# Kernel optimization log

Hardware: AMD Instinct MI355X
Metric: run time of the kernel (lower is better)

Reference implementation:

```python
import jax, jax.numpy as jnp
import numpy as np

N_USERS = 100000
N_ITEMS = 50000
D = 64
L = 3          # TopKformer_layers
E = 1000000    # number of train (user,item) edges


def setup_inputs() -> dict:
    key = jax.random.key(0)
    k1, k2, k3, k4, k5 = jax.random.split(key, 5)
    return {
        "users_w": jax.random.normal(k1, (N_USERS, D), jnp.float32) * 0.1,
        "items_w": jax.random.normal(k2, (N_ITEMS, D), jnp.float32) * 0.1,
        "beta_w": jax.random.normal(k3, (N_USERS, L), jnp.float32),
        "train_user": jax.random.randint(k4, (E,), 0, N_USERS, dtype=jnp.int32),
        "train_item": jax.random.randint(k5, (E,), 0, N_ITEMS, dtype=jnp.int32),
    }


def reference(users_w, items_w, beta_w, train_user, train_item):
    """Model.computer(): LightGCN-style bipartite propagation where each
    layer's user update is gated by a learned per-user beta = tanh(beta_w).
    Returns concat([user_embs, item_embs]) after L propagation layers."""
    beta = jnp.tanh(beta_w)  # [N_USERS, L], as in Model.beta_value

    # symmetric degree normalization 1/sqrt(d_u * d_i) over train edges
    ones = jnp.ones(train_user.shape[0], users_w.dtype)
    du = jnp.clip(jax.ops.segment_sum(ones, train_user, N_USERS), 1.0)
    di = jnp.clip(jax.ops.segment_sum(ones, train_item, N_ITEMS), 1.0)
    norm = (1.0 / jnp.sqrt(du[train_user] * di[train_item]))[:, None]  # [E,1]

    u_emb, i_emb = users_w, items_w
    for l in range(L):
        # gather neighbor embeddings along edges, scatter-add back (irregular access)
        msg_u = jax.ops.segment_sum(i_emb[train_item] * norm, train_user, N_USERS)
        msg_i = jax.ops.segment_sum(u_emb[train_user] * norm, train_item, N_ITEMS)
        u_emb = msg_u + beta[:, l:l + 1] * u_emb  # beta-weighted residual (per user)
        i_emb = msg_i
    return jnp.concatenate([u_emb, i_emb], axis=0)  # [N_USERS+N_ITEMS, D]
```

## Files before the change

kernel.cpp:

```cpp
#include <hip/hip_runtime.h>

#define NUSERS 100000
#define NITEMS 50000
#define NV (NUSERS + NITEMS)
#define DIM 64
#define NLAYERS 3
#define PAD 64
#define BINSHIFT 9
#define BINSZ 512
#define NBINS ((NV + BINSZ - 1) / BINSZ)
#define EPB 1024

typedef _Float16 half4v __attribute__((ext_vector_type(4)));
typedef _Float16 half8v __attribute__((ext_vector_type(8)));

__global__ void hist_kernel(const int* __restrict__ tu, const int* __restrict__ ti,
                            int* __restrict__ cnt, int E) {
    __shared__ int h[NBINS];
    int t = threadIdx.x, b = blockIdx.x;
    for (int i = t; i < NBINS; i += 256) h[i] = 0;
    __syncthreads();
    int base = b * EPB;
#pragma unroll
    for (int j = 0; j < 4; ++j) {
        int e = base + t + 256 * j;
        if (e < E) {
            atomicAdd(&h[tu[e] >> BINSHIFT], 1);
            atomicAdd(&h[(NUSERS + ti[e]) >> BINSHIFT], 1);
        }
    }
    __syncthreads();
    for (int i = t; i < NBINS; i += 256) cnt[(size_t)b * NBINS + i] = h[i];
}

__global__ void colscan_kernel(int* __restrict__ cnt, int* __restrict__ bintot, int nblk) {
    __shared__ int sh[256];
    int bin = blockIdx.x, t = threadIdx.x;
    int chunk = (nblk + 255) / 256;
    int v[8];
    int sum = 0;
    for (int j = 0; j < chunk; ++j) {
        int blk = t * chunk + j;
        v[j] = (blk < nblk) ? cnt[(size_t)blk * NBINS + bin] : 0;
        sum += v[j];
    }
    sh[t] = sum;
    __syncthreads();
    for (int d = 1; d < 256; d <<= 1) {
        int x = (t >= d) ? sh[t - d] : 0;
        __syncthreads();
        sh[t] += x;
        __syncthreads();
    }
    int run = sh[t] - sum;
    for (int j = 0; j < chunk; ++j) {
        int blk = t * chunk + j;
        if (blk < nblk) { cnt[(size_t)blk * NBINS + bin] = run; run += v[j]; }
    }
    if (t == 255) bintot[bin] = sh[255];
}

__global__ void binscan_kernel(const int* __restrict__ bintot, int* __restrict__ binstart) {
    __shared__ int sh[512];
    int t = threadIdx.x;
    int v = (t < NBINS) ? bintot[t] : 0;
    sh[t] = v;
    __syncthreads();
    for (int d = 1; d < 512; d <<= 1) {
        int x = (t >= d) ? sh[t - d] : 0;
        __syncthreads();
        sh[t] += x;
        __syncthreads();
    }
    if (t < NBINS) binstart[t] = sh[t] - v;
    if (t == NBINS - 1) binstart[NBINS] = sh[t];
}

__global__ void scatter_kernel(const int* __restrict__ tu, const int* __restrict__ ti,
                               const int* __restrict__ cnt, const int* __restrict__ binstart,
                               unsigned int* __restrict__ binbuf, int E) {
    __shared__ int h[NBINS];
    __shared__ int bb[NBINS];
    __shared__ int bs[NBINS];
    int t = threadIdx.x, b = blockIdx.x;
    for (int i = t; i < NBINS; i += 256) {
        h[i] = 0;
        bb[i] = cnt[(size_t)b * NBINS + i];
        bs[i] = binstart[i];
    }
    __syncthreads();
    int base = b * EPB;
#pragma unroll
    for (int j = 0; j < 4; ++j) {
        int e = base + t + 256 * j;
        if (e < E) {
            int u = tu[e];
            int w = NUSERS + ti[e];
            int bu = u >> BINSHIFT, bw = w >> BINSHIFT;
            int r1 = atomicAdd(&h[bu], 1);
            int r2 = atomicAdd(&h[bw], 1);
            binbuf[bs[bu] + bb[bu] + r1] = ((unsigned)(u & (BINSZ - 1)) << 18) | (unsigned)w;
            binbuf[bs[bw] + bb[bw] + r2] = ((unsigned)(w & (BINSZ - 1)) << 18) | (unsigned)u;
        }
    }
}

__global__ void bfill_kernel(const unsigned int* __restrict__ binbuf,
                             const int* __restrict__ binstart,
                             int* __restrict__ deg, int* __restrict__ adj) {
    __shared__ int c[BINSZ];
    int bin = blockIdx.x, t = threadIdx.x;
    c[t] = 0;
    __syncthreads();
    int start = binstart[bin];
    int n = binstart[bin + 1] - start;
    int vbase = bin << BINSHIFT;
    for (int k = t; k < n; k += 512) {
        unsigned rec = binbuf[start + k];
        int vloc = rec >> 18;
        int nbr = (int)(rec & 0x3FFFFu);
        int r = atomicAdd(&c[vloc], 1);
        adj[((vbase + vloc) << 6) + r] = nbr << 7;
    }
    __syncthreads();
    int v = vbase + t;
    if (v < NV) deg[v] = c[t];
}

__global__ void init_kernel(const float* __restrict__ users_w, const float* __restrict__ items_w,
                            const int* __restrict__ deg, _Float16* __restrict__ Yh) {
    int t = blockIdx.x * blockDim.x + threadIdx.x;
    int n4 = NV * (DIM / 4);
    if (t >= n4) return;
    int v = t >> 4;
    float r = rsqrtf(fmaxf((float)deg[v], 1.0f));
    const float4* src = (v < NUSERS)
        ? reinterpret_cast<const float4*>(users_w) + t
        : reinterpret_cast<const float4*>(items_w) + (t - NUSERS * (DIM / 4));
    float4 x = *src;
    half4v h;
    h.x = (_Float16)(x.x * r);
    h.y = (_Float16)(x.y * r);
    h.z = (_Float16)(x.z * r);
    h.w = (_Float16)(x.w * r);
    reinterpret_cast<half4v*>(Yh)[t] = h;
}

template <bool FINAL>
__global__ void gather_kernel(const _Float16* __restrict__ Yh, const int* __restrict__ deg,
                              const int* __restrict__ adj,
                              const float* __restrict__ beta_w,
                              void* __restrict__ dst_v, int layer) {
    int wid = (blockIdx.x * blockDim.x + threadIdx.x) >> 6;
    int lane = threadIdx.x & 63;
    if (wid >= NV) return;
    int g = lane >> 3;
    int p = lane & 7;
    int s = wid << 6;
    const char* rowb = (const char*)Yh + p * 16;
    const int NVS = NV << 7;

    int dg = deg[wid];
    int raw0 = __builtin_nontemporal_load(&adj[s + g]);
    int raw1 = __builtin_nontemporal_load(&adj[s + 8 + g]);
    int raw2 = __builtin_nontemporal_load(&adj[s + 16 + g]);
    int raw3 = __builtin_nontemporal_load(&adj[s + 24 + g]);
    bool isU = wid < NUSERS;
    float bw_ = 0.f;
    half8v hy = {};
    if (isU && g == 0) {
        bw_ = beta_w[wid * NLAYERS + layer];
        hy = *reinterpret_cast<const half8v*>(Yh + (size_t)wid * DIM + p * 8);
    }

    int o0 = (g      < dg) ? raw0 : NVS;
    int o1 = (8 + g  < dg) ? raw1 : NVS;
    int o2 = (16 + g < dg) ? raw2 : NVS;
    int o3 = (24 + g < dg) ? raw3 : NVS;
    half8v h0 = *reinterpret_cast<const half8v*>(rowb + (size_t)(unsigned)o0);
    half8v h1 = *reinterpret_cast<const half8v*>(rowb + (size_t)(unsigned)o1);
    half8v h2 = *reinterpret_cast<const half8v*>(rowb + (size_t)(unsigned)o2);
    half8v h3 = *reinterpret_cast<const half8v*>(rowb + (size_t)(unsigned)o3);

    half8v hs = (h0 + h1) + (h2 + h3);
    float a[8];
#pragma unroll
    for (int j = 0; j < 8; ++j) a[j] = (float)hs[j];

    if (dg > 32) {
#pragma unroll
        for (int jb = 0; jb < 4; ++jb) {
            int slotbase = 32 + jb * 8;
            if (slotbase < dg) {
                int ks = slotbase + g;
                int rw = __builtin_nontemporal_load(&adj[s + ks]);
                int oj = (ks < dg) ? rw : NVS;
                half8v hj = *reinterpret_cast<const half8v*>(rowb + (size_t)(unsigned)oj);
#pragma unroll
                for (int j = 0; j < 8; ++j) a[j] += (float)hj[j];
            }
        }
    }

#pragma unroll
    for (int j = 0; j < 8; ++j) a[j] += __shfl_xor(a[j], 8);
#pragma unroll
    for (int j = 0; j < 8; ++j) a[j] += __shfl_xor(a[j], 16);
#pragma unroll
    for (int j = 0; j < 8; ++j) a[j] += __shfl_xor(a[j], 32);

    if (g == 0) {
        float fdg = fmaxf((float)dg, 1.0f);
        float r = rsqrtf(fdg);
        float b = isU ? tanhf(bw_) : 0.f;
        if (!FINAL) {
            float rr = r * r;
            half8v o;
#pragma unroll
            for (int j = 0; j < 8; ++j) o[j] = (_Float16)(rr * a[j] + b * (float)hy[j]);
            reinterpret_cast<half8v*>((_Float16*)dst_v + (size_t)wid * DIM)[p] = o;
        } else {
            float c = b * __builtin_sqrtf(fdg);
            float4 o0f, o1f;
            o0f.x = r * a[0] + c * (float)hy[0];
            o0f.y = r * a[1] + c * (float)hy[1];
            o0f.z = r * a[2] + c * (float)hy[2];
            o0f.w = r * a[3] + c * (float)hy[3];
            o1f.x = r * a[4] + c * (float)hy[4];
            o1f.y = r * a[5] + c * (float)hy[5];
            o1f.z = r * a[6] + c * (float)hy[6];
            o1f.w = r * a[7] + c * (float)hy[7];
            float4* dp = reinterpret_cast<float4*>((float*)dst_v + (size_t)wid * DIM + p * 8);
            dp[0] = o0f;
            dp[1] = o1f;
        }
    }
}

extern "C" void kernel_launch(void* const* d_in, const int* in_sizes, int n_in,
                              void* d_out, int out_size, void* d_ws, size_t ws_size,
                              hipStream_t stream) {
    const float* users_w = (const float*)d_in[0];
    const float* items_w = (const float*)d_in[1];
    const float* beta_w  = (const float*)d_in[2];
    const int*   tu      = (const int*)d_in[3];
    const int*   ti      = (const int*)d_in[4];
    const int    E       = in_sizes[3];
    float*       out     = (float*)d_out;

    int nblk = (E + EPB - 1) / EPB;

    char* ws = (char*)d_ws;
    size_t woff = 0;
    auto take = [&](size_t bytes) {
        char* p = ws + woff;
        woff += (bytes + 1023) & ~(size_t)1023;
        return p;
    };
    int*      deg      = (int*)take((size_t)NV * sizeof(int));
    int*      cnt      = (int*)take((size_t)nblk * NBINS * sizeof(int));
    int*      bintot   = (int*)take((size_t)NBINS * sizeof(int));
    int*      binstart = (int*)take((size_t)(NBINS + 1) * sizeof(int));
    unsigned* binbuf   = (unsigned*)take((size_t)2 * E * sizeof(unsigned));
    int*      adj      = (int*)take((size_t)NV * PAD * sizeof(int));
    _Float16* Yh0      = (_Float16*)take((size_t)(NV + 1) * DIM * sizeof(_Float16));

    _Float16* Dh = (_Float16*)d_out;

    const int blk = 256;

    hist_kernel<<<nblk, 256, 0, stream>>>(tu, ti, cnt, E);
    colscan_kernel<<<NBINS, 256, 0, stream>>>(cnt, bintot, nblk);
    binscan_kernel<<<1, 512, 0, stream>>>(bintot, binstart);
    scatter_kernel<<<nblk, 256, 0, stream>>>(tu, ti, cnt, binstart, binbuf, E);
    bfill_kernel<<<NBINS, 512, 0, stream>>>(binbuf, binstart, deg, adj);

    int n4 = NV * (DIM / 4);
    init_kernel<<<(n4 + blk - 1) / blk, blk, 0, stream>>>(users_w, items_w, deg, Yh0);
    hipMemsetAsync(Yh0 + (size_t)NV * DIM, 0, DIM * sizeof(_Float16), stream);
    hipMemsetAsync(Dh + (size_t)NV * DIM, 0, DIM * sizeof(_Float16), stream);

    int gblocks = ((size_t)NV * 64 + blk - 1) / blk;

    gather_kernel<false><<<gblocks, blk, 0, stream>>>(Yh0, deg, adj, beta_w, Dh, 0);
    gather_kernel<false><<<gblocks, blk, 0, stream>>>(Dh, deg, adj, beta_w, Yh0, 1);
    gather_kernel<true ><<<gblocks, blk, 0, stream>>>(Yh0, deg, adj, beta_w, out, 2);
}
```

Before: 210.1 us.

## Fold pad-row memsets into init kernel, skip upper gathers for low degree

The two hipMemsetAsync calls that zero the sentinel pad rows of Yh0 and Dh are folded into extra threads of init_kernel, which removes two operations from the stream. In the gather kernel the third and fourth neighbor loads are skipped when a vertex has degree at most 16. The adjacency loads also switch from nontemporal to normal cached loads. These cut launch count and wasted sentinel-row traffic, at the cost of a divergent branch and different cache behaviour for adj.

```diff
diff --git a/kernel.cpp b/kernel.cpp
--- a/kernel.cpp
+++ b/kernel.cpp
@@ -128,10 +128,16 @@
 }
 
 __global__ void init_kernel(const float* __restrict__ users_w, const float* __restrict__ items_w,
-                            const int* __restrict__ deg, _Float16* __restrict__ Yh) {
+                            const int* __restrict__ deg, _Float16* __restrict__ Yh,
+                            _Float16* __restrict__ Dh) {
     int t = blockIdx.x * blockDim.x + threadIdx.x;
     int n4 = NV * (DIM / 4);
-    if (t >= n4) return;
+    if (t >= n4) {
+        int z = t - n4;
+        if (z < 16) reinterpret_cast<half4v*>(Yh + (size_t)NV * DIM)[z] = half4v{};
+        else if (z < 32) reinterpret_cast<half4v*>(Dh + (size_t)NV * DIM)[z - 16] = half4v{};
+        return;
+    }
     int v = t >> 4;
     float r = rsqrtf(fmaxf((float)deg[v], 1.0f));
     const float4* src = (v < NUSERS)
@@ -161,10 +167,10 @@
     const int NVS = NV << 7;
 
     int dg = deg[wid];
-    int raw0 = __builtin_nontemporal_load(&adj[s + g]);
-    int raw1 = __builtin_nontemporal_load(&adj[s + 8 + g]);
-    int raw2 = __builtin_nontemporal_load(&adj[s + 16 + g]);
-    int raw3 = __builtin_nontemporal_load(&adj[s + 24 + g]);
+    int raw0 = adj[s + g];
+    int raw1 = adj[s + 8 + g];
+    int raw2 = adj[s + 16 + g];
+    int raw3 = adj[s + 24 + g];
     bool isU = wid < NUSERS;
     float bw_ = 0.f;
     half8v hy = {};
@@ -175,14 +181,19 @@
 
     int o0 = (g      < dg) ? raw0 : NVS;
     int o1 = (8 + g  < dg) ? raw1 : NVS;
-    int o2 = (16 + g < dg) ? raw2 : NVS;
-    int o3 = (24 + g < dg) ? raw3 : NVS;
     half8v h0 = *reinterpret_cast<const half8v*>(rowb + (size_t)(unsigned)o0);
     half8v h1 = *reinterpret_cast<const half8v*>(rowb + (size_t)(unsigned)o1);
-    half8v h2 = *reinterpret_cast<const half8v*>(rowb + (size_t)(unsigned)o2);
-    half8v h3 = *reinterpret_cast<const half8v*>(rowb + (size_t)(unsigned)o3);
-
-    half8v hs = (h0 + h1) + (h2 + h3);
+
+    half8v hs;
+    if (dg > 16) {
+        int o2 = (16 + g < dg) ? raw2 : NVS;
+        int o3 = (24 + g < dg) ? raw3 : NVS;
+        half8v h2 = *reinterpret_cast<const half8v*>(rowb + (size_t)(unsigned)o2);
+        half8v h3 = *reinterpret_cast<const half8v*>(rowb + (size_t)(unsigned)o3);
+        hs = (h0 + h1) + (h2 + h3);
+    } else {
+        hs = h0 + h1;
+    }
     float a[8];
 #pragma unroll
     for (int j = 0; j < 8; ++j) a[j] = (float)hs[j];
@@ -193,7 +204,7 @@
             int slotbase = 32 + jb * 8;
             if (slotbase < dg) {
                 int ks = slotbase + g;
-                int rw = __builtin_nontemporal_load(&adj[s + ks]);
+                int rw = adj[s + ks];
                 int oj = (ks < dg) ? rw : NVS;
                 half8v hj = *reinterpret_cast<const half8v*>(rowb + (size_t)(unsigned)oj);
 #pragma unroll
@@ -276,9 +287,7 @@
     bfill_kernel<<<NBINS, 512, 0, stream>>>(binbuf, binstart, deg, adj);
 
     int n4 = NV * (DIM / 4);
-    init_kernel<<<(n4 + blk - 1) / blk, blk, 0, stream>>>(users_w, items_w, deg, Yh0);
-    hipMemsetAsync(Yh0 + (size_t)NV * DIM, 0, DIM * sizeof(_Float16), stream);
-    hipMemsetAsync(Dh + (size_t)NV * DIM, 0, DIM * sizeof(_Float16), stream);
+    init_kernel<<<(n4 + 32 + blk - 1) / blk, blk, 0, stream>>>(users_w, items_w, deg, Yh0, Dh);
 
     int gblocks = ((size_t)NV * 64 + blk - 1) / blk;
 
```

Result: faster. 191.5 us (-8.8%).
